# Performance work log

Measured on AMD Instinct MI355X. Metric: run time of the kernel, lower is better.

## Reference

```python
import jax, jax.numpy as jnp
import numpy as np

B, H, W = 2, 64, 64
C = 19          # num_classes
D = 64          # embed_dim
NH = 4          # num_heads
E = 4           # num_experts
HD = 128        # hidden_dim = 2*D
EPS = 1e-5


def setup_inputs() -> dict:
    key = jax.random.key(0)
    ks = jax.random.split(key, 12)
    n = lambda k, shape, s=0.02: jax.random.normal(k, shape, jnp.float32) * s
    z = lambda shape: jnp.zeros(shape, jnp.float32)
    o = lambda shape: jnp.ones(shape, jnp.float32)
    return {
        "depth_map": jax.random.normal(ks[0], (B, 1, H, W), jnp.float32),
        "prob_map": jax.nn.softmax(jax.random.normal(ks[1], (B, C, H, W), jnp.float32), axis=1),
        "emb_w": n(ks[2], (1 + C, D)), "emb_b": z((D,)),            # 1x1 conv == per-pixel linear
        "in_proj_w": n(ks[3], (D, 3 * D)), "in_proj_b": z((3 * D,)),
        "attn_out_w": n(ks[4], (D, D)), "attn_out_b": z((D,)),
        "ln1_g": o((D,)), "ln1_b": z((D,)),
        "ln2_g": o((D,)), "ln2_b": z((D,)),
        "exp_w1": n(ks[5], (E, D, HD)), "exp_b1": z((E, HD)),
        "exp_w2": n(ks[6], (E, HD, D)), "exp_b2": z((E, D)),
        "gate_w": n(ks[7], (D, E)), "gate_b": z((E,)),
        "proj_w": n(ks[8], (D, 1)), "proj_b": z((1,)),
    }


def _layernorm(x, g, b):
    m = jnp.mean(x, axis=-1, keepdims=True)
    v = jnp.mean(jnp.square(x - m), axis=-1, keepdims=True)
    return (x - m) * jax.lax.rsqrt(v + EPS) * g + b


def reference(depth_map, prob_map, emb_w, emb_b, in_proj_w, in_proj_b,
              attn_out_w, attn_out_b, ln1_g, ln1_b, ln2_g, ln2_b,
              exp_w1, exp_b1, exp_w2, exp_b2, gate_w, gate_b, proj_w, proj_b):
    Bv, _, Hv, Wv = depth_map.shape
    N = Hv * Wv
    dh = D // NH

    x = jnp.concatenate([depth_map, prob_map], axis=1)            # [B, 1+C, H, W]
    # 1x1 conv embedding -> token sequence [B, N, D]
    x_seq = (jnp.einsum('bchw,cd->bhwd', x, emb_w) + emb_b).reshape(Bv, N, D)

    # pre-norm self-attention
    xn = _layernorm(x_seq, ln1_g, ln1_b)
    qkv = xn @ in_proj_w + in_proj_b                              # [B, N, 3D]
    q, k, v = jnp.split(qkv, 3, axis=-1)
    q = q.reshape(Bv, N, NH, dh)
    k = k.reshape(Bv, N, NH, dh)
    v = v.reshape(Bv, N, NH, dh)
    scores = jnp.einsum('bqhd,bkhd->bhqk', q, k) / np.sqrt(dh).astype(np.float32)
    attn = jax.nn.softmax(scores, axis=-1)
    o = jnp.einsum('bhqk,bkhd->bqhd', attn, v).reshape(Bv, N, D)
    attn_out = o @ attn_out_w + attn_out_b
    x_att = x_seq + attn_out

    # soft MoE over all tokens
    xn2 = _layernorm(x_att, ln2_g, ln2_b)
    gw = jax.nn.softmax(xn2 @ gate_w + gate_b, axis=-1)           # [B, N, E]
    h1 = jax.nn.relu(jnp.einsum('bnd,edh->bneh', xn2, exp_w1) + exp_b1)
    eo = jnp.einsum('bneh,ehd->bned', h1, exp_w2) + exp_b2        # [B, N, E, D]
    combined = jnp.einsum('bned,bne->bnd', eo, gw)
    x_out = x_att + combined

    weight_seq = x_out @ proj_w + proj_b                          # [B, N, 1]
    return jax.nn.sigmoid(weight_seq.reshape(Bv, 1, Hv, Wv))
```

## Files before the change

### kernel.cpp

```cpp
#include <hip/hip_runtime.h>
#include <math.h>

#define DEV __device__ __forceinline__

namespace {

constexpr int Bb  = 2;
constexpr int Nn  = 4096;
constexpr int Cc  = 19;
constexpr int NHh = 4;
constexpr int Ee  = 4;
constexpr float EPSv = 1e-5f;

typedef __attribute__((ext_vector_type(4))) short short4v;
typedef __attribute__((ext_vector_type(8))) short short8v;
typedef __attribute__((ext_vector_type(4))) float f32x4;
typedef unsigned short ushort_t;
typedef unsigned int uint_t;

constexpr size_t OFF_XSEQ = 0;
constexpr size_t OFF_XATT = OFF_XSEQ + (size_t)Bb*Nn*64;
constexpr size_t OFF_OATT = OFF_XATT + (size_t)Bb*Nn*64;
constexpr size_t OFF_QB   = OFF_OATT + (size_t)Bb*Nn*64;
constexpr size_t OFF_KB   = OFF_QB + (size_t)Bb*Nn*32/2;
constexpr size_t OFF_VB   = OFF_KB + (size_t)Bb*Nn*32/2;
constexpr size_t OFF_VT   = OFF_VB + (size_t)Bb*Nn*32/2;

DEV float wredsum(float x) {
  #pragma unroll
  for (int off = 32; off > 0; off >>= 1) x += __shfl_xor(x, off, 64);
  return x;
}
DEV ushort_t f2bf(float x) {
  uint_t u = __builtin_bit_cast(uint_t, x);
  u += 0x7fffu + ((u >> 16) & 1u);
  return (ushort_t)(u >> 16);
}
DEV uint_t pk2(float a, float b) {
  return (uint_t)f2bf(a) | ((uint_t)f2bf(b) << 16);
}

__global__ __launch_bounds__(256) void k_embed_qkv(
    const float* __restrict__ depth, const float* __restrict__ prob,
    const float* __restrict__ emb_w, const float* __restrict__ emb_b,
    const float* __restrict__ ipw,   const float* __restrict__ ipb,
    const float* __restrict__ ln1g,  const float* __restrict__ ln1b,
    float* __restrict__ ws)
{
  const int lane = threadIdx.x & 63;
  const int wid  = threadIdx.x >> 6;
  const int tok  = blockIdx.x * 4 + wid;
  const int b = tok >> 12, n = tok & (Nn - 1);
  const int d = lane;

  float acc = emb_b[d];
  acc += depth[(size_t)b * Nn + n] * emb_w[d];
  #pragma unroll
  for (int c = 0; c < Cc; ++c)
    acc += prob[((size_t)b * Cc + c) * Nn + n] * emb_w[(1 + c) * 64 + d];

  ws[OFF_XSEQ + (size_t)tok * 64 + d] = acc;

  float mean = wredsum(acc) * (1.f / 64.f);
  float diff = acc - mean;
  float var  = wredsum(diff * diff) * (1.f / 64.f);
  float xn   = diff * rsqrtf(var + EPSv) * ln1g[d] + ln1b[d];

  float aq = ipb[d], ak = ipb[64 + d], av = ipb[128 + d];
  #pragma unroll 8
  for (int j = 0; j < 64; ++j) {
    float xj = __shfl(xn, j, 64);
    const float* wr = ipw + j * 192;
    aq = fmaf(xj, wr[d],       aq);
    ak = fmaf(xj, wr[64 + d],  ak);
    av = fmaf(xj, wr[128 + d], av);
  }
  const int h = d >> 4, dd = d & 15;
  ushort_t* qb = (ushort_t*)(ws + OFF_QB);
  ushort_t* kb = (ushort_t*)(ws + OFF_KB);
  ushort_t* vb = (ushort_t*)(ws + OFF_VB);
  const size_t base = ((size_t)(b * NHh + h) * Nn + n) * 16 + dd;
  qb[base] = f2bf(aq * 0.25f);
  kb[base] = f2bf(ak);
  vb[base] = f2bf(av);
}

__global__ __launch_bounds__(256) void k_transpose_v(float* __restrict__ ws)
{
  __shared__ ushort_t tile[256][17];
  const ushort_t* vb = (const ushort_t*)(ws + OFF_VB);
  ushort_t*       vt = (ushort_t*)(ws + OFF_VT);
  const int bh = blockIdx.y;
  const int n0 = blockIdx.x * 256;
  const int t  = threadIdx.x;

  const ushort_t* src = vb + ((size_t)bh * Nn + n0 + t) * 16;
  short8v r0 = *(const short8v*)(src);
  short8v r1 = *(const short8v*)(src + 8);
  #pragma unroll
  for (int i = 0; i < 8; ++i) { tile[t][i] = (ushort_t)r0[i]; tile[t][8 + i] = (ushort_t)r1[i]; }
  __syncthreads();

  const int d = t & 15, seg = t >> 4;
  short8v w0, w1;
  #pragma unroll
  for (int i = 0; i < 8; ++i) {
    w0[i] = (short)tile[seg * 16 + i][d];
    w1[i] = (short)tile[seg * 16 + 8 + i][d];
  }
  ushort_t* dst = vt + ((size_t)bh * 16 + d) * Nn + n0 + seg * 16;
  *(short8v*)(dst)     = w0;
  *(short8v*)(dst + 8) = w1;
}

__global__ __launch_bounds__(256) void k_attn_mfma(float* __restrict__ ws)
{
  const int lane = threadIdx.x & 63;
  const int wid  = threadIdx.x >> 6;
  const int blk  = blockIdx.x;
  const int bh   = blk >> 6;
  const int qt   = (blk & 63) * 4 + wid;
  const int q0   = qt * 16;
  const int g    = lane >> 4;
  const int qi   = lane & 15;

  const ushort_t* qb = (const ushort_t*)(ws + OFF_QB) + (size_t)bh * Nn * 16;
  const ushort_t* kb = (const ushort_t*)(ws + OFF_KB) + (size_t)bh * Nn * 16;
  const ushort_t* vt = (const ushort_t*)(ws + OFF_VT) + (size_t)bh * 16 * Nn;
  float* oatt = ws + OFF_OATT;

  short8v qf = {};
  if (lane < 32)
    qf = *(const short8v*)(qb + (size_t)(q0 + qi) * 16 + g * 8);

  f32x4 O = {0.f, 0.f, 0.f, 0.f};
  float mrun = -INFINITY, lrun = 0.f;
  const f32x4 z4 = {0.f, 0.f, 0.f, 0.f};
  const ushort_t* vrow = vt + (size_t)qi * Nn;

  #pragma unroll 2
  for (int c = 0; c < Nn / 64; ++c) {
    const int kb0 = c * 64;
    short8v kf0 = {}, kf1 = {}, kf2 = {}, kf3 = {};
    if (lane < 32) {
      const ushort_t* kr = kb + (size_t)(kb0 + qi) * 16 + g * 8;
      kf0 = *(const short8v*)(kr);
      kf1 = *(const short8v*)(kr + 256);
      kf2 = *(const short8v*)(kr + 512);
      kf3 = *(const short8v*)(kr + 768);
    }
    const ushort_t* vr = vrow + kb0 + 4 * g;
    short4v va00 = *(const short4v*)(vr);
    short4v va01 = *(const short4v*)(vr + 16);
    short4v va10 = *(const short4v*)(vr + 32);
    short4v va11 = *(const short4v*)(vr + 48);

    f32x4 s0 = __builtin_amdgcn_mfma_f32_16x16x32_bf16(kf0, qf, z4, 0, 0, 0);
    f32x4 s1 = __builtin_amdgcn_mfma_f32_16x16x32_bf16(kf1, qf, z4, 0, 0, 0);
    f32x4 s2 = __builtin_amdgcn_mfma_f32_16x16x32_bf16(kf2, qf, z4, 0, 0, 0);
    f32x4 s3 = __builtin_amdgcn_mfma_f32_16x16x32_bf16(kf3, qf, z4, 0, 0, 0);

    float cm = fmaxf(fmaxf(fmaxf(s0[0], s0[1]), fmaxf(s0[2], s0[3])),
                     fmaxf(fmaxf(s1[0], s1[1]), fmaxf(s1[2], s1[3])));
    cm = fmaxf(cm, fmaxf(fmaxf(s2[0], s2[1]), fmaxf(s2[2], s2[3])));
    cm = fmaxf(cm, fmaxf(fmaxf(s3[0], s3[1]), fmaxf(s3[2], s3[3])));
    cm = fmaxf(cm, __shfl_xor(cm, 16, 64));
    cm = fmaxf(cm, __shfl_xor(cm, 32, 64));

    if (!__all(cm <= mrun + 8.f)) {
      const float nm = fmaxf(mrun, cm);
      const float c2 = __expf(mrun - nm);
      lrun *= c2;
      O[0] *= c2; O[1] *= c2; O[2] *= c2; O[3] *= c2;
      mrun = nm;
    }

    float p[16];
    #pragma unroll
    for (int r = 0; r < 4; ++r) {
      p[r]      = __expf(s0[r] - mrun);
      p[4 + r]  = __expf(s1[r] - mrun);
      p[8 + r]  = __expf(s2[r] - mrun);
      p[12 + r] = __expf(s3[r] - mrun);
    }
    float ps = 0.f;
    #pragma unroll
    for (int i = 0; i < 16; ++i) ps += p[i];
    ps += __shfl_xor(ps, 16, 64);
    ps += __shfl_xor(ps, 32, 64);
    lrun += ps;

    union { short8v v; uint_t w[4]; } P0, P1;
    P0.w[0] = pk2(p[0], p[1]);   P0.w[1] = pk2(p[2], p[3]);
    P0.w[2] = pk2(p[4], p[5]);   P0.w[3] = pk2(p[6], p[7]);
    P1.w[0] = pk2(p[8], p[9]);   P1.w[1] = pk2(p[10], p[11]);
    P1.w[2] = pk2(p[12], p[13]); P1.w[3] = pk2(p[14], p[15]);

    union { short8v v; short4v hh[2]; } VA0, VA1;
    VA0.hh[0] = va00; VA0.hh[1] = va01;
    VA1.hh[0] = va10; VA1.hh[1] = va11;

    O = __builtin_amdgcn_mfma_f32_16x16x32_bf16(VA0.v, P0.v, O, 0, 0, 0);
    O = __builtin_amdgcn_mfma_f32_16x16x32_bf16(VA1.v, P1.v, O, 0, 0, 0);
  }

  const float rl = 1.f / lrun;
  const int b = bh >> 2, h = bh & 3;
  float4 ov = make_float4(O[0] * rl, O[1] * rl, O[2] * rl, O[3] * rl);
  *(float4*)(oatt + ((size_t)b * Nn + q0 + qi) * 64 + h * 16 + g * 4) = ov;
}

__global__ __launch_bounds__(256) void k_out_proj(
    const float* __restrict__ aow, const float* __restrict__ aob,
    float* __restrict__ ws)
{
  const int lane = threadIdx.x & 63;
  const int wid  = threadIdx.x >> 6;
  const int tok  = blockIdx.x * 4 + wid;

  const float o = ws[OFF_OATT + (size_t)tok * 64 + lane];
  float acc = aob[lane];
  #pragma unroll 8
  for (int j = 0; j < 64; ++j)
    acc = fmaf(__shfl(o, j, 64), aow[j * 64 + lane], acc);
  const size_t xi = (size_t)tok * 64 + lane;
  ws[OFF_XATT + xi] = ws[OFF_XSEQ + xi] + acc;
}

constexpr int RT = 4;

__global__ __launch_bounds__(256) void k_moe(
    const float* __restrict__ ln2g, const float* __restrict__ ln2b,
    const float* __restrict__ w1,   const float* __restrict__ b1,
    const float* __restrict__ w2,   const float* __restrict__ b2,
    const float* __restrict__ gwt,  const float* __restrict__ gbt,
    const float* __restrict__ pw,   const float* __restrict__ pbv,
    const float* __restrict__ ws,   float* __restrict__ out)
{
  __shared__ float xn2T[4][64][RT];
  __shared__ float h1T[4][128][RT];
  __shared__ float gwS[4][RT][Ee];

  const int lane = threadIdx.x & 63;
  const int wid  = threadIdx.x >> 6;
  const int tok0 = (blockIdx.x * 4 + wid) * RT;
  const int d = lane;
  const float* xatt = ws + OFF_XATT;

  float xar[RT], comb[RT];
  #pragma unroll
  for (int ti = 0; ti < RT; ++ti) {
    const float xa = xatt[(size_t)(tok0 + ti) * 64 + d];
    xar[ti] = xa;
    comb[ti] = 0.f;
    float mean = wredsum(xa) * (1.f / 64.f);
    float diff = xa - mean;
    float var  = wredsum(diff * diff) * (1.f / 64.f);
    float xn   = diff * rsqrtf(var + EPSv) * ln2g[d] + ln2b[d];
    xn2T[wid][d][ti] = xn;

    float ge[Ee];
    #pragma unroll
    for (int e = 0; e < Ee; ++e) ge[e] = xn * gwt[d * Ee + e];
    #pragma unroll
    for (int off = 32; off > 0; off >>= 1) {
      #pragma unroll
      for (int e = 0; e < Ee; ++e) ge[e] += __shfl_xor(ge[e], off, 64);
    }
    #pragma unroll
    for (int e = 0; e < Ee; ++e) ge[e] += gbt[e];
    float gm = fmaxf(fmaxf(ge[0], ge[1]), fmaxf(ge[2], ge[3]));
    float gs = 0.f;
    #pragma unroll
    for (int e = 0; e < Ee; ++e) { ge[e] = __expf(ge[e] - gm); gs += ge[e]; }
    if (lane == 0) {
      #pragma unroll
      for (int e = 0; e < Ee; ++e) gwS[wid][ti][e] = ge[e] / gs;
    }
  }

  for (int e = 0; e < Ee; ++e) {
    const float* w1e = w1 + (size_t)e * 64 * 128;
    const float* w2e = w2 + (size_t)e * 128 * 64;
    float a0[RT], a1[RT];
    const float bb0 = b1[e * 128 + lane], bb1 = b1[e * 128 + 64 + lane];
    #pragma unroll
    for (int ti = 0; ti < RT; ++ti) { a0[ti] = bb0; a1[ti] = bb1; }
    #pragma unroll 4
    for (int j = 0; j < 64; ++j) {
      const float4 xv = *(const float4*)&xn2T[wid][j][0];
      const float wa = w1e[j * 128 + lane];
      const float wb = w1e[j * 128 + 64 + lane];
      a0[0] = fmaf(xv.x, wa, a0[0]); a0[1] = fmaf(xv.y, wa, a0[1]);
      a0[2] = fmaf(xv.z, wa, a0[2]); a0[3] = fmaf(xv.w, wa, a0[3]);
      a1[0] = fmaf(xv.x, wb, a1[0]); a1[1] = fmaf(xv.y, wb, a1[1]);
      a1[2] = fmaf(xv.z, wb, a1[2]); a1[3] = fmaf(xv.w, wb, a1[3]);
    }
    #pragma unroll
    for (int ti = 0; ti < RT; ++ti) {
      h1T[wid][lane][ti]      = fmaxf(a0[ti], 0.f);
      h1T[wid][64 + lane][ti] = fmaxf(a1[ti], 0.f);
    }
    float ac[RT];
    const float bb2 = b2[e * 64 + lane];
    #pragma unroll
    for (int ti = 0; ti < RT; ++ti) ac[ti] = bb2;
    #pragma unroll 4
    for (int j = 0; j < 128; ++j) {
      const float4 hv = *(const float4*)&h1T[wid][j][0];
      const float wv = w2e[j * 64 + lane];
      ac[0] = fmaf(hv.x, wv, ac[0]); ac[1] = fmaf(hv.y, wv, ac[1]);
      ac[2] = fmaf(hv.z, wv, ac[2]); ac[3] = fmaf(hv.w, wv, ac[3]);
    }
    #pragma unroll
    for (int ti = 0; ti < RT; ++ti)
      comb[ti] = fmaf(gwS[wid][ti][e], ac[ti], comb[ti]);
  }

  const float pb0 = pbv[0];
  #pragma unroll
  for (int ti = 0; ti < RT; ++ti) {
    const float xo = xar[ti] + comb[ti];
    float r = xo * pw[d];
    r = wredsum(r);
    if (lane == 0)
      out[tok0 + ti] = 1.f / (1.f + __expf(-(r + pb0)));
  }
}

}

extern "C" void kernel_launch(void* const* d_in, const int* in_sizes, int n_in,
                              void* d_out, int out_size, void* d_ws, size_t ws_size,
                              hipStream_t stream) {
  const float* depth = (const float*)d_in[0];
  const float* prob  = (const float*)d_in[1];
  const float* emb_w = (const float*)d_in[2];
  const float* emb_b = (const float*)d_in[3];
  const float* ipw   = (const float*)d_in[4];
  const float* ipb   = (const float*)d_in[5];
  const float* aow   = (const float*)d_in[6];
  const float* aob   = (const float*)d_in[7];
  const float* ln1g  = (const float*)d_in[8];
  const float* ln1b  = (const float*)d_in[9];
  const float* ln2g  = (const float*)d_in[10];
  const float* ln2b  = (const float*)d_in[11];
  const float* w1    = (const float*)d_in[12];
  const float* b1    = (const float*)d_in[13];
  const float* w2    = (const float*)d_in[14];
  const float* b2    = (const float*)d_in[15];
  const float* gatew = (const float*)d_in[16];
  const float* gateb = (const float*)d_in[17];
  const float* projw = (const float*)d_in[18];
  const float* projb = (const float*)d_in[19];
  float* out = (float*)d_out;
  float* wsf = (float*)d_ws;

  k_embed_qkv<<<Bb * Nn / 4, 256, 0, stream>>>(depth, prob, emb_w, emb_b,
                                               ipw, ipb, ln1g, ln1b, wsf);
  k_transpose_v<<<dim3(Nn / 256, Bb * NHh), 256, 0, stream>>>(wsf);
  k_attn_mfma<<<Bb * NHh * 64, 256, 0, stream>>>(wsf);
  k_out_proj<<<Bb * Nn / 4, 256, 0, stream>>>(aow, aob, wsf);
  k_moe<<<Bb * Nn / (4 * RT), 256, 0, stream>>>(ln2g, ln2b, w1, b1, w2, b2,
                                                gatew, gateb, projw, projb,
                                                wsf, out);
}
```

Measured before the change: 257.2 us.

## Split attention over key halves and stage weights in shared memory

Attention now splits the key range into two segments on a second grid dimension and writes partial max, sum and output, which the out-projection kernel merges flash-decoding style. This doubles the attention wave count, since 512 blocks is low occupancy on this GPU. Softmax switches to exp2 with log2e folded into Q, and a hardware packed bf16 conversion replaces software rounding. The QKV, out-projection and MoE kernels also stage their weights in LDS. This costs extra partial-result traffic, more synchronisation, and per-expert reloads of 64KB of weights into shared memory, which limits MoE occupancy.

```diff
diff --git a/kernel.cpp b/kernel.cpp
--- a/kernel.cpp
+++ b/kernel.cpp
@@ -11,6 +11,7 @@
 constexpr int NHh = 4;
 constexpr int Ee  = 4;
 constexpr float EPSv = 1e-5f;
+constexpr float LOG2E = 1.4426950408889634f;
 
 typedef __attribute__((ext_vector_type(4))) short short4v;
 typedef __attribute__((ext_vector_type(8))) short short8v;
@@ -18,13 +19,16 @@
 typedef unsigned short ushort_t;
 typedef unsigned int uint_t;
 
+constexpr size_t QKV_F    = (size_t)Bb * Nn * 32;
 constexpr size_t OFF_XSEQ = 0;
 constexpr size_t OFF_XATT = OFF_XSEQ + (size_t)Bb*Nn*64;
-constexpr size_t OFF_OATT = OFF_XATT + (size_t)Bb*Nn*64;
-constexpr size_t OFF_QB   = OFF_OATT + (size_t)Bb*Nn*64;
-constexpr size_t OFF_KB   = OFF_QB + (size_t)Bb*Nn*32/2;
-constexpr size_t OFF_VB   = OFF_KB + (size_t)Bb*Nn*32/2;
-constexpr size_t OFF_VT   = OFF_VB + (size_t)Bb*Nn*32/2;
+constexpr size_t OFF_QB   = OFF_XATT + (size_t)Bb*Nn*64;
+constexpr size_t OFF_KB   = OFF_QB + QKV_F;
+constexpr size_t OFF_VB   = OFF_KB + QKV_F;
+constexpr size_t OFF_VT   = OFF_VB + QKV_F;
+constexpr size_t OFF_MP   = OFF_VT + QKV_F;
+constexpr size_t OFF_LP   = OFF_MP + (size_t)Bb*NHh*2*Nn;
+constexpr size_t OFF_OP   = OFF_LP + (size_t)Bb*NHh*2*Nn;
 
 DEV float wredsum(float x) {
   #pragma unroll
@@ -36,8 +40,10 @@
   u += 0x7fffu + ((u >> 16) & 1u);
   return (ushort_t)(u >> 16);
 }
-DEV uint_t pk2(float a, float b) {
-  return (uint_t)f2bf(a) | ((uint_t)f2bf(b) << 16);
+DEV uint_t cvtpk(float a, float b) {
+  uint_t r;
+  asm("v_cvt_pk_bf16_f32 %0, %1, %2" : "=v"(r) : "v"(a), "v"(b));
+  return r;
 }
 
 __global__ __launch_bounds__(256) void k_embed_qkv(
@@ -47,8 +53,17 @@
     const float* __restrict__ ln1g,  const float* __restrict__ ln1b,
     float* __restrict__ ws)
 {
-  const int lane = threadIdx.x & 63;
-  const int wid  = threadIdx.x >> 6;
+  __shared__ float ipws[64 * 192];
+
+  const int t = threadIdx.x;
+  #pragma unroll
+  for (int i = 0; i < 12; ++i) {
+    const int idx = (i * 256 + t) * 4;
+    *(float4*)&ipws[idx] = *(const float4*)&ipw[idx];
+  }
+
+  const int lane = t & 63;
+  const int wid  = t >> 6;
   const int tok  = blockIdx.x * 4 + wid;
   const int b = tok >> 12, n = tok & (Nn - 1);
   const int d = lane;
@@ -66,11 +81,13 @@
   float var  = wredsum(diff * diff) * (1.f / 64.f);
   float xn   = diff * rsqrtf(var + EPSv) * ln1g[d] + ln1b[d];
 
+  __syncthreads();
+
   float aq = ipb[d], ak = ipb[64 + d], av = ipb[128 + d];
   #pragma unroll 8
   for (int j = 0; j < 64; ++j) {
     float xj = __shfl(xn, j, 64);
-    const float* wr = ipw + j * 192;
+    const float* wr = ipws + j * 192;
     aq = fmaf(xj, wr[d],       aq);
     ak = fmaf(xj, wr[64 + d],  ak);
     av = fmaf(xj, wr[128 + d], av);
@@ -80,7 +97,7 @@
   ushort_t* kb = (ushort_t*)(ws + OFF_KB);
   ushort_t* vb = (ushort_t*)(ws + OFF_VB);
   const size_t base = ((size_t)(b * NHh + h) * Nn + n) * 16 + dd;
-  qb[base] = f2bf(aq * 0.25f);
+  qb[base] = f2bf(aq * 0.25f * LOG2E);
   kb[base] = f2bf(ak);
   vb[base] = f2bf(av);
 }
@@ -118,6 +135,7 @@
   const int lane = threadIdx.x & 63;
   const int wid  = threadIdx.x >> 6;
   const int blk  = blockIdx.x;
+  const int seg  = blockIdx.y;
   const int bh   = blk >> 6;
   const int qt   = (blk & 63) * 4 + wid;
   const int q0   = qt * 16;
@@ -127,7 +145,6 @@
   const ushort_t* qb = (const ushort_t*)(ws + OFF_QB) + (size_t)bh * Nn * 16;
   const ushort_t* kb = (const ushort_t*)(ws + OFF_KB) + (size_t)bh * Nn * 16;
   const ushort_t* vt = (const ushort_t*)(ws + OFF_VT) + (size_t)bh * 16 * Nn;
-  float* oatt = ws + OFF_OATT;
 
   short8v qf = {};
   if (lane < 32)
@@ -138,8 +155,9 @@
   const f32x4 z4 = {0.f, 0.f, 0.f, 0.f};
   const ushort_t* vrow = vt + (size_t)qi * Nn;
 
+  const int c0 = seg * 32;
   #pragma unroll 2
-  for (int c = 0; c < Nn / 64; ++c) {
+  for (int c = c0; c < c0 + 32; ++c) {
     const int kb0 = c * 64;
     short8v kf0 = {}, kf1 = {}, kf2 = {}, kf3 = {};
     if (lane < 32) {
@@ -167,9 +185,9 @@
     cm = fmaxf(cm, __shfl_xor(cm, 16, 64));
     cm = fmaxf(cm, __shfl_xor(cm, 32, 64));
 
-    if (!__all(cm <= mrun + 8.f)) {
+    if (!__all(cm <= mrun + 11.5f)) {
       const float nm = fmaxf(mrun, cm);
-      const float c2 = __expf(mrun - nm);
+      const float c2 = exp2f(mrun - nm);
       lrun *= c2;
       O[0] *= c2; O[1] *= c2; O[2] *= c2; O[3] *= c2;
       mrun = nm;
@@ -178,10 +196,10 @@
     float p[16];
     #pragma unroll
     for (int r = 0; r < 4; ++r) {
-      p[r]      = __expf(s0[r] - mrun);
-      p[4 + r]  = __expf(s1[r] - mrun);
-      p[8 + r]  = __expf(s2[r] - mrun);
-      p[12 + r] = __expf(s3[r] - mrun);
+      p[r]      = exp2f(s0[r] - mrun);
+      p[4 + r]  = exp2f(s1[r] - mrun);
+      p[8 + r]  = exp2f(s2[r] - mrun);
+      p[12 + r] = exp2f(s3[r] - mrun);
     }
     float ps = 0.f;
     #pragma unroll
@@ -191,10 +209,10 @@
     lrun += ps;
 
     union { short8v v; uint_t w[4]; } P0, P1;
-    P0.w[0] = pk2(p[0], p[1]);   P0.w[1] = pk2(p[2], p[3]);
-    P0.w[2] = pk2(p[4], p[5]);   P0.w[3] = pk2(p[6], p[7]);
-    P1.w[0] = pk2(p[8], p[9]);   P1.w[1] = pk2(p[10], p[11]);
-    P1.w[2] = pk2(p[12], p[13]); P1.w[3] = pk2(p[14], p[15]);
+    P0.w[0] = cvtpk(p[0], p[1]);   P0.w[1] = cvtpk(p[2], p[3]);
+    P0.w[2] = cvtpk(p[4], p[5]);   P0.w[3] = cvtpk(p[6], p[7]);
+    P1.w[0] = cvtpk(p[8], p[9]);   P1.w[1] = cvtpk(p[10], p[11]);
+    P1.w[2] = cvtpk(p[12], p[13]); P1.w[3] = cvtpk(p[14], p[15]);
 
     union { short8v v; short4v hh[2]; } VA0, VA1;
     VA0.hh[0] = va00; VA0.hh[1] = va01;
@@ -204,25 +222,47 @@
     O = __builtin_amdgcn_mfma_f32_16x16x32_bf16(VA1.v, P1.v, O, 0, 0, 0);
   }
 
-  const float rl = 1.f / lrun;
-  const int b = bh >> 2, h = bh & 3;
-  float4 ov = make_float4(O[0] * rl, O[1] * rl, O[2] * rl, O[3] * rl);
-  *(float4*)(oatt + ((size_t)b * Nn + q0 + qi) * 64 + h * 16 + g * 4) = ov;
+  const size_t pb = ((size_t)bh * 2 + seg) * Nn + q0 + qi;
+  if (g == 0) { ws[OFF_MP + pb] = mrun; ws[OFF_LP + pb] = lrun; }
+  f32x4* op = (f32x4*)(ws + OFF_OP + pb * 16 + g * 4);
+  *op = O;
 }
 
 __global__ __launch_bounds__(256) void k_out_proj(
     const float* __restrict__ aow, const float* __restrict__ aob,
     float* __restrict__ ws)
 {
-  const int lane = threadIdx.x & 63;
-  const int wid  = threadIdx.x >> 6;
+  __shared__ float aows[64 * 64];
+  const int t = threadIdx.x;
+  #pragma unroll
+  for (int i = 0; i < 4; ++i) {
+    const int idx = (i * 256 + t) * 4;
+    *(float4*)&aows[idx] = *(const float4*)&aow[idx];
+  }
+
+  const int lane = t & 63;
+  const int wid  = t >> 6;
   const int tok  = blockIdx.x * 4 + wid;
-
-  const float o = ws[OFF_OATT + (size_t)tok * 64 + lane];
+  const int b = tok >> 12, n = tok & (Nn - 1);
+  const int h = lane >> 4, dd = lane & 15;
+  const int bh = b * NHh + h;
+
+  const size_t p0 = ((size_t)bh * 2 + 0) * Nn + n;
+  const size_t p1 = p0 + Nn;
+  const float m0 = ws[OFF_MP + p0], m1 = ws[OFF_MP + p1];
+  const float l0 = ws[OFF_LP + p0], l1 = ws[OFF_LP + p1];
+  const float M  = fmaxf(m0, m1);
+  const float c0 = exp2f(m0 - M), c1 = exp2f(m1 - M);
+  const float o0 = ws[OFF_OP + p0 * 16 + dd];
+  const float o1 = ws[OFF_OP + p1 * 16 + dd];
+  const float o  = (c0 * o0 + c1 * o1) / (c0 * l0 + c1 * l1);
+
+  __syncthreads();
+
   float acc = aob[lane];
   #pragma unroll 8
   for (int j = 0; j < 64; ++j)
-    acc = fmaf(__shfl(o, j, 64), aow[j * 64 + lane], acc);
+    acc = fmaf(__shfl(o, j, 64), aows[j * 64 + lane], acc);
   const size_t xi = (size_t)tok * 64 + lane;
   ws[OFF_XATT + xi] = ws[OFF_XSEQ + xi] + acc;
 }
@@ -240,6 +280,8 @@
   __shared__ float xn2T[4][64][RT];
   __shared__ float h1T[4][128][RT];
   __shared__ float gwS[4][RT][Ee];
+  __shared__ float w1s[64 * 128];
+  __shared__ float w2s[128 * 64];
 
   const int lane = threadIdx.x & 63;
   const int wid  = threadIdx.x >> 6;
@@ -280,8 +322,20 @@
   }
 
   for (int e = 0; e < Ee; ++e) {
-    const float* w1e = w1 + (size_t)e * 64 * 128;
-    const float* w2e = w2 + (size_t)e * 128 * 64;
+    __syncthreads();
+    {
+      const int t = threadIdx.x;
+      const float* w1e = w1 + (size_t)e * 8192;
+      const float* w2e = w2 + (size_t)e * 8192;
+      #pragma unroll
+      for (int i = 0; i < 8; ++i) {
+        const int idx = (i * 256 + t) * 4;
+        *(float4*)&w1s[idx] = *(const float4*)&w1e[idx];
+        *(float4*)&w2s[idx] = *(const float4*)&w2e[idx];
+      }
+    }
+    __syncthreads();
+
     float a0[RT], a1[RT];
     const float bb0 = b1[e * 128 + lane], bb1 = b1[e * 128 + 64 + lane];
     #pragma unroll
@@ -289,8 +343,8 @@
     #pragma unroll 4
     for (int j = 0; j < 64; ++j) {
       const float4 xv = *(const float4*)&xn2T[wid][j][0];
-      const float wa = w1e[j * 128 + lane];
-      const float wb = w1e[j * 128 + 64 + lane];
+      const float wa = w1s[j * 128 + lane];
+      const float wb = w1s[j * 128 + 64 + lane];
       a0[0] = fmaf(xv.x, wa, a0[0]); a0[1] = fmaf(xv.y, wa, a0[1]);
       a0[2] = fmaf(xv.z, wa, a0[2]); a0[3] = fmaf(xv.w, wa, a0[3]);
       a1[0] = fmaf(xv.x, wb, a1[0]); a1[1] = fmaf(xv.y, wb, a1[1]);
@@ -308,7 +362,7 @@
     #pragma unroll 4
     for (int j = 0; j < 128; ++j) {
       const float4 hv = *(const float4*)&h1T[wid][j][0];
-      const float wv = w2e[j * 64 + lane];
+      const float wv = w2s[j * 64 + lane];
       ac[0] = fmaf(hv.x, wv, ac[0]); ac[1] = fmaf(hv.y, wv, ac[1]);
       ac[2] = fmaf(hv.z, wv, ac[2]); ac[3] = fmaf(hv.w, wv, ac[3]);
     }
@@ -359,7 +413,7 @@
   k_embed_qkv<<<Bb * Nn / 4, 256, 0, stream>>>(depth, prob, emb_w, emb_b,
                                                ipw, ipb, ln1g, ln1b, wsf);
   k_transpose_v<<<dim3(Nn / 256, Bb * NHh), 256, 0, stream>>>(wsf);
-  k_attn_mfma<<<Bb * NHh * 64, 256, 0, stream>>>(wsf);
+  k_attn_mfma<<<dim3(Bb * NHh * 64, 2), 256, 0, stream>>>(wsf);
   k_out_proj<<<Bb * Nn / 4, 256, 0, stream>>>(aow, aob, wsf);
   k_moe<<<Bb * Nn / (4 * RT), 256, 0, stream>>>(ln2g, ln2b, w1, b1, w2, b2,
                                                 gatew, gateb, projw, projb,
```

After: 236.7 us. 8.0% less time.
